# Optimization experiments

Measured on AMD Instinct MI355X. Metric: run time of the kernel, lower is better.

## Reference

```python
import jax, jax.numpy as jnp
import numpy as np

N_NODES = 100000


def _gcn_layer(h, W, b, src, dst, norm, n):
    # h: [N, Fin] -> transform then normalized scatter-add aggregation
    h = h @ W                                   # [N, Fout]
    msg = h[src] * norm[:, None]                # [E', Fout] gather + scale
    out = jax.ops.segment_sum(msg, dst, num_segments=n)  # scatter-add
    return out + b


def setup_inputs() -> dict:
    key = jax.random.key(0)
    k1, k2, k3, k4 = jax.random.split(key, 4)
    N, F_IN, HID, C, E = N_NODES, 512, 128, 40, 1600000
    x = jax.random.normal(k1, (N, F_IN), dtype=jnp.float32)
    edge_index = jax.random.randint(k2, (2, E), 0, N, dtype=jnp.int64)
    W1 = jax.random.normal(k3, (F_IN, HID), dtype=jnp.float32) * (1.0 / np.sqrt(F_IN))
    b1 = jnp.zeros((HID,), dtype=jnp.float32)
    W2 = jax.random.normal(k4, (HID, C), dtype=jnp.float32) * (1.0 / np.sqrt(HID))
    b2 = jnp.zeros((C,), dtype=jnp.float32)
    return {"x": x, "edge_index": edge_index, "W1": W1, "b1": b1, "W2": W2, "b2": b2}


def reference(x, edge_index, W1, b1, W2, b2):
    n = x.shape[0]
    # add self-loops (GCNConv default)
    loop = jnp.arange(n, dtype=edge_index.dtype)
    src = jnp.concatenate([edge_index[0], loop])
    dst = jnp.concatenate([edge_index[1], loop])
    # symmetric normalization: deg counted on destination (in-degree, incl. self-loop)
    deg = jax.ops.segment_sum(jnp.ones_like(dst, dtype=x.dtype), dst, num_segments=n)
    dis = jnp.where(deg > 0, jax.lax.rsqrt(deg), 0.0)  # deg^{-1/2}
    norm = dis[src] * dis[dst]                          # per-edge weight

    h = jax.nn.relu(_gcn_layer(x, W1, b1, src, dst, norm, n))
    # dropout: identity in eval mode (training=False)
    h = _gcn_layer(h, W2, b2, src, dst, norm, n)
    return jax.nn.log_softmax(h, axis=1)
```

## Files before the change

### kernel.cpp

```cpp
#include <hip/hip_runtime.h>
#include <hip/hip_bf16.h>


#define F_IN 512
#define HID  128
#define NC   40
#define NCP  48

typedef __attribute__((ext_vector_type(8))) short bf16x8;
typedef __attribute__((ext_vector_type(4))) float f32x4v;

__device__ __forceinline__ ushort f2bf(float f) {
    unsigned r;
    asm("v_cvt_pk_bf16_f32 %0, %1, %1" : "=v"(r) : "v"(f));
    return (ushort)r;
}
__device__ __forceinline__ unsigned cvtpk(float a, float b) {
    unsigned r;
    asm("v_cvt_pk_bf16_f32 %0, %1, %2" : "=v"(r) : "v"(a), "v"(b));
    return r;
}
__device__ __forceinline__ float bf2f(ushort u) {
    return __uint_as_float((unsigned)u << 16);
}
__device__ __forceinline__ bf16x8 cvt8(float4 lo, float4 hi) {
    union { unsigned u[4]; bf16x8 v; } t;
    t.u[0] = cvtpk(lo.x, lo.y); t.u[1] = cvtpk(lo.z, lo.w);
    t.u[2] = cvtpk(hi.x, hi.y); t.u[3] = cvtpk(hi.z, hi.w);
    return t.v;
}

__global__ void prep_k(const int* __restrict__ dst, int E, int EB,
                       unsigned* __restrict__ cnt,
                       const float* __restrict__ W1, const float* __restrict__ W2,
                       ushort* __restrict__ W1p, ushort* __restrict__ W2p) {
    int b = blockIdx.x;
    if (b < EB) {
        int t = b * 256 + threadIdx.x;
        if (t < E) atomicAdd(&cnt[dst[t]], 1u);
        return;
    }
    int t = (b - EB) * 256 + threadIdx.x;
    if (t < 65536) {
        int j = t & 7, n = (t >> 3) & 127, kb = (t >> 10) & 3, s = t >> 12;
        int k = s * 32 + kb * 8 + j;
        W1p[t] = f2bf(W1[(size_t)k * HID + n]);
    } else {
        int q = t - 65536;
        if (q < 6144) {
            int j = q & 7;
            int i2 = q >> 3;
            int n = i2 % 48;
            int i3 = i2 / 48;
            int kb = i3 & 3, ks = i3 >> 2;
            int k = ks * 32 + kb * 8 + j;
            float v = (n < NC) ? W2[(size_t)k * NC + n] : 0.f;
            W2p[q] = f2bf(v);
        }
    }
}

__global__ __launch_bounds__(1024) void scan_block(const unsigned* __restrict__ cnt,
                                                   unsigned* __restrict__ offs,
                                                   unsigned* __restrict__ bsums,
                                                   float* __restrict__ dis, int N) {
    int tid = threadIdx.x;
    int i = blockIdx.x * 1024 + tid;
    unsigned v = (i < N) ? cnt[i] : 0u;
    if (i < N) dis[i] = rsqrtf((float)v + 1.0f);
    int lane = tid & 63, w = tid >> 6;
    unsigned s = v;
    #pragma unroll
    for (int d = 1; d < 64; d <<= 1) {
        unsigned t = __shfl_up(s, d, 64);
        if (lane >= d) s += t;
    }
    __shared__ unsigned wt[16];
    if (lane == 63) wt[w] = s;
    __syncthreads();
    unsigned add = 0;
    #pragma unroll
    for (int j = 0; j < 16; j++) add += (j < w) ? wt[j] : 0u;
    unsigned incl = s + add;
    if (i < N) offs[i] = incl - v;
    if (tid == 1023) bsums[blockIdx.x] = incl;
}

__global__ __launch_bounds__(1024) void scan_add2(unsigned* __restrict__ offs,
                                                  const unsigned* __restrict__ bsums,
                                                  int N, unsigned total) {
    int i = blockIdx.x * 1024 + threadIdx.x;
    int lane = threadIdx.x & 63;
    unsigned s = 0;
    for (int j = lane; j < (int)blockIdx.x; j += 64) s += bsums[j];
    #pragma unroll
    for (int d = 1; d < 64; d <<= 1) s += __shfl_xor(s, d, 64);
    if (i < N) offs[i] += s;
    if (i == 0) offs[N] = total;
}

__global__ __launch_bounds__(256) void fill_gemm1(
        const int* __restrict__ src, const int* __restrict__ dst,
        const unsigned* __restrict__ offs, unsigned* __restrict__ cursor,
        int* __restrict__ col, int E, int GB,
        const float* __restrict__ A, const ushort* __restrict__ Bp,
        const float* __restrict__ dis, ushort* __restrict__ C, int N) {
    if (blockIdx.x >= GB) {
        int t = (blockIdx.x - GB) * 256 + threadIdx.x;
        if (t < E) {
            int s = src[t], d = dst[t];
            unsigned pos = offs[d] + atomicAdd(&cursor[d], 1u);
            col[pos] = s;
        }
        return;
    }
    const int tid  = threadIdx.x;
    const int wave = tid >> 6;
    const int lane = tid & 63;
    const int quad = lane >> 4;
    const int mr   = lane & 15;
    const int base = (blockIdx.x * 4 + wave) * 32;
    if (base >= N) return;
    const int r0 = base + mr;
    const int r1 = base + 16 + mr;
    const bool ok0 = r0 < N, ok1 = r1 < N;
    const float* ap0 = A + (size_t)(ok0 ? r0 : 0) * F_IN + quad * 8;
    const float* ap1 = A + (size_t)(ok1 ? r1 : 0) * F_IN + quad * 8;
    const ushort* bp = Bp + quad * 1024 + mr * 8;

    f32x4v acc0[8], acc1[8];
    #pragma unroll
    for (int t = 0; t < 8; t++) {
        acc0[t] = (f32x4v){0.f, 0.f, 0.f, 0.f};
        acc1[t] = (f32x4v){0.f, 0.f, 0.f, 0.f};
    }

    float4 av[2][4];
    #pragma unroll
    for (int b = 0; b < 2; b++) {
        av[b][0] = *(const float4*)(ap0 + b * 32);
        av[b][1] = *(const float4*)(ap0 + b * 32 + 4);
        av[b][2] = *(const float4*)(ap1 + b * 32);
        av[b][3] = *(const float4*)(ap1 + b * 32 + 4);
    }

    for (int s = 0; s < 16; s++) {
        bf16x8 fa0 = cvt8(av[s & 1][0], av[s & 1][1]);
        bf16x8 fa1 = cvt8(av[s & 1][2], av[s & 1][3]);
        if (s < 14) {
            av[s & 1][0] = *(const float4*)(ap0 + (s + 2) * 32);
            av[s & 1][1] = *(const float4*)(ap0 + (s + 2) * 32 + 4);
            av[s & 1][2] = *(const float4*)(ap1 + (s + 2) * 32);
            av[s & 1][3] = *(const float4*)(ap1 + (s + 2) * 32 + 4);
        }
        const ushort* bs = bp + s * 4096;
        #pragma unroll
        for (int t = 0; t < 8; t++) {
            bf16x8 b = *(const bf16x8*)(bs + t * 128);
            acc0[t] = __builtin_amdgcn_mfma_f32_16x16x32_bf16(fa0, b, acc0[t], 0, 0, 0);
            acc1[t] = __builtin_amdgcn_mfma_f32_16x16x32_bf16(fa1, b, acc1[t], 0, 0, 0);
        }
    }

    #pragma unroll
    for (int rr = 0; rr < 4; rr++) {
        int ra = base + quad * 4 + rr;
        if (ra < N) {
            float ds = dis[ra];
            #pragma unroll
            for (int t = 0; t < 8; t++)
                C[(size_t)ra * HID + t * 16 + mr] = f2bf(acc0[t][rr] * ds);
        }
        int rb = base + 16 + quad * 4 + rr;
        if (rb < N) {
            float ds = dis[rb];
            #pragma unroll
            for (int t = 0; t < 8; t++)
                C[(size_t)rb * HID + t * 16 + mr] = f2bf(acc1[t][rr] * ds);
        }
    }
}

__global__ __launch_bounds__(256) void agg1_k(const ushort* __restrict__ h,
                                              const int* __restrict__ col,
                                              const unsigned* __restrict__ offs,
                                              const float* __restrict__ dis,
                                              const float* __restrict__ b1,
                                              ushort* __restrict__ out, int N) {
    int node = blockIdx.x * 4 + (threadIdx.x >> 6);
    if (node >= N) return;
    int lane = threadIdx.x & 63;
    int ni = lane >> 4;
    int fl = lane & 15;
    const ushort* hb = h + (size_t)fl * 8;
    float a[8] = {0.f, 0.f, 0.f, 0.f, 0.f, 0.f, 0.f, 0.f};
    if (ni == 0) {
        uint4 v = *(const uint4*)(hb + (size_t)node * HID);
        const ushort* u = (const ushort*)&v;
        #pragma unroll
        for (int j = 0; j < 8; j++) a[j] = bf2f(u[j]);
    }
    unsigned p0 = offs[node], p1 = offs[node + 1];
    int sA = (p0 + ni     < p1) ? col[p0 + ni]     : -1;
    int sB = (p0 + ni + 4 < p1) ? col[p0 + ni + 4] : -1;
    for (unsigned p = p0; p < p1; p += 8) {
        int sC = (p + 8 + ni  < p1) ? col[p + 8 + ni]  : -1;
        int sD = (p + 12 + ni < p1) ? col[p + 12 + ni] : -1;
        if (sA >= 0) {
            uint4 v = *(const uint4*)(hb + (size_t)sA * HID);
            const ushort* u = (const ushort*)&v;
            #pragma unroll
            for (int j = 0; j < 8; j++) a[j] += bf2f(u[j]);
        }
        if (sB >= 0) {
            uint4 v = *(const uint4*)(hb + (size_t)sB * HID);
            const ushort* u = (const ushort*)&v;
            #pragma unroll
            for (int j = 0; j < 8; j++) a[j] += bf2f(u[j]);
        }
        sA = sC; sB = sD;
    }
    #pragma unroll
    for (int j = 0; j < 8; j++) {
        a[j] += __shfl_xor(a[j], 16);
        a[j] += __shfl_xor(a[j], 32);
    }
    if (ni == 0) {
        float dd = dis[node];
        float4 bb0 = *(const float4*)(b1 + fl * 8);
        float4 bb1 = *(const float4*)(b1 + fl * 8 + 4);
        const float bb[8] = {bb0.x, bb0.y, bb0.z, bb0.w, bb1.x, bb1.y, bb1.z, bb1.w};
        __align__(16) ushort o[8];
        #pragma unroll
        for (int j = 0; j < 8; j++) o[j] = f2bf(fmaxf(a[j] * dd + bb[j], 0.f));
        *(uint4*)(out + (size_t)node * HID + (size_t)fl * 8) = *(const uint4*)o;
    }
}

__global__ __launch_bounds__(256) void gemm2_mfma(const ushort* __restrict__ A,
                                                  const ushort* __restrict__ W2p,
                                                  const float* __restrict__ dis,
                                                  ushort* __restrict__ h2, int N) {
    const int tid  = threadIdx.x;
    const int wave = tid >> 6;
    const int lane = tid & 63;
    const int quad = lane >> 4;
    const int mr   = lane & 15;
    const int base = (blockIdx.x * 4 + wave) * 32;
    if (base >= N) return;
    const int r0 = base + mr;
    const int r1 = base + 16 + mr;
    const bool ok0 = r0 < N, ok1 = r1 < N;
    const ushort* ap0 = A + (size_t)(ok0 ? r0 : 0) * HID + quad * 8;
    const ushort* ap1 = A + (size_t)(ok1 ? r1 : 0) * HID + quad * 8;
    const ushort* bp = W2p + quad * 384 + mr * 8;

    f32x4v acc0[3], acc1[3];
    #pragma unroll
    for (int t = 0; t < 3; t++) {
        acc0[t] = (f32x4v){0.f, 0.f, 0.f, 0.f};
        acc1[t] = (f32x4v){0.f, 0.f, 0.f, 0.f};
    }
    #pragma unroll
    for (int ks = 0; ks < 4; ks++) {
        bf16x8 a0 = *(const bf16x8*)(ap0 + ks * 32);
        bf16x8 a1 = *(const bf16x8*)(ap1 + ks * 32);
        #pragma unroll
        for (int t = 0; t < 3; t++) {
            bf16x8 b = *(const bf16x8*)(bp + ks * 1536 + t * 128);
            acc0[t] = __builtin_amdgcn_mfma_f32_16x16x32_bf16(a0, b, acc0[t], 0, 0, 0);
            acc1[t] = __builtin_amdgcn_mfma_f32_16x16x32_bf16(a1, b, acc1[t], 0, 0, 0);
        }
    }
    #pragma unroll
    for (int rr = 0; rr < 4; rr++) {
        int ra = base + quad * 4 + rr;
        if (ra < N) {
            float ds = dis[ra];
            #pragma unroll
            for (int t = 0; t < 3; t++) {
                int c = t * 16 + mr;
                if (c < NC) h2[(size_t)ra * NCP + c] = f2bf(acc0[t][rr] * ds);
            }
        }
        int rb = base + 16 + quad * 4 + rr;
        if (rb < N) {
            float ds = dis[rb];
            #pragma unroll
            for (int t = 0; t < 3; t++) {
                int c = t * 16 + mr;
                if (c < NC) h2[(size_t)rb * NCP + c] = f2bf(acc1[t][rr] * ds);
            }
        }
    }
}

__global__ __launch_bounds__(256) void agg2_ls(const ushort* __restrict__ h2,
                                               const int* __restrict__ col,
                                               const unsigned* __restrict__ offs,
                                               const float* __restrict__ dis,
                                               const float* __restrict__ b2,
                                               float* __restrict__ out, int N) {
    int node = blockIdx.x * 4 + (threadIdx.x >> 6);
    if (node >= N) return;
    int lane = threadIdx.x & 63;
    int ni = lane >> 3;
    int fl = lane & 7;
    const bool act = fl < 5;
    const ushort* hb = h2 + (size_t)fl * 8;
    float a[8] = {0.f, 0.f, 0.f, 0.f, 0.f, 0.f, 0.f, 0.f};
    if (ni == 0 && act) {
        uint4 v = *(const uint4*)(hb + (size_t)node * NCP);
        const ushort* u = (const ushort*)&v;
        #pragma unroll
        for (int j = 0; j < 8; j++) a[j] = bf2f(u[j]);
    }
    unsigned p0 = offs[node], p1 = offs[node + 1];
    int sA = (p0 + ni     < p1) ? col[p0 + ni]     : -1;
    int sB = (p0 + ni + 8 < p1) ? col[p0 + ni + 8] : -1;
    for (unsigned p = p0; p < p1; p += 16) {
        int sC = (p + 16 + ni < p1) ? col[p + 16 + ni] : -1;
        int sD = (p + 24 + ni < p1) ? col[p + 24 + ni] : -1;
        if (sA >= 0 && act) {
            uint4 v = *(const uint4*)(hb + (size_t)sA * NCP);
            const ushort* u = (const ushort*)&v;
            #pragma unroll
            for (int j = 0; j < 8; j++) a[j] += bf2f(u[j]);
        }
        if (sB >= 0 && act) {
            uint4 v = *(const uint4*)(hb + (size_t)sB * NCP);
            const ushort* u = (const ushort*)&v;
            #pragma unroll
            for (int j = 0; j < 8; j++) a[j] += bf2f(u[j]);
        }
        sA = sC; sB = sD;
    }
    #pragma unroll
    for (int j = 0; j < 8; j++) {
        a[j] += __shfl_xor(a[j], 8);
        a[j] += __shfl_xor(a[j], 16);
        a[j] += __shfl_xor(a[j], 32);
    }
    float dd = dis[node];
    float l[8];
    float m = -1e30f;
    if (act) {
        #pragma unroll
        for (int j = 0; j < 8; j++) {
            l[j] = a[j] * dd + b2[fl * 8 + j];
            m = fmaxf(m, l[j]);
        }
    }
    #pragma unroll
    for (int d = 1; d < 8; d <<= 1) m = fmaxf(m, __shfl_xor(m, d, 8));
    float s = 0.f;
    if (act) {
        #pragma unroll
        for (int j = 0; j < 8; j++) s += __expf(l[j] - m);
    }
    #pragma unroll
    for (int d = 1; d < 8; d <<= 1) s += __shfl_xor(s, d, 8);
    float lse = m + __logf(s);
    if (ni == 0 && act) {
        float* op = out + (size_t)node * NC + fl * 8;
        *(float4*)op       = make_float4(l[0]-lse, l[1]-lse, l[2]-lse, l[3]-lse);
        *(float4*)(op + 4) = make_float4(l[4]-lse, l[5]-lse, l[6]-lse, l[7]-lse);
    }
}

extern "C" void kernel_launch(void* const* d_in, const int* in_sizes, int n_in,
                              void* d_out, int out_size, void* d_ws, size_t ws_size,
                              hipStream_t stream) {
    const float* x  = (const float*)d_in[0];
    const int*   ei = (const int*)d_in[1];
    const float* W1 = (const float*)d_in[2];
    const float* b1 = (const float*)d_in[3];
    const float* W2 = (const float*)d_in[4];
    const float* b2 = (const float*)d_in[5];
    float* out = (float*)d_out;

    const int N = in_sizes[0] / F_IN;
    const int E = in_sizes[1] / 2;
    const int* src = ei;
    const int* dst = ei + E;

    char* ws = (char*)d_ws;
    size_t o = 0;
    unsigned* cnt  = (unsigned*)(ws + o); o += (size_t)N * 4;
    unsigned* cur  = (unsigned*)(ws + o); o += (size_t)N * 4;
    float*    dis  = (float*)   (ws + o); o += (size_t)N * 4;
    unsigned* offs = (unsigned*)(ws + o); o += (size_t)(N + 4) * 4;
    unsigned* bsums= (unsigned*)(ws + o); o += 4096;
    int*      col  = (int*)     (ws + o); o += (size_t)E * 4;
    o = (o + 15) & ~(size_t)15;
    ushort*   W1p  = (ushort*)  (ws + o); o += (size_t)F_IN * HID * 2;
    o = (o + 15) & ~(size_t)15;
    ushort*   W2p  = (ushort*)  (ws + o); o += 6144 * 2;
    o = (o + 15) & ~(size_t)15;
    ushort*   h1   = (ushort*)  (ws + o); o += (size_t)N * HID * 2;
    o = (o + 15) & ~(size_t)15;
    ushort*   ag1  = (ushort*)  (ws + o); o += (size_t)N * HID * 2;
    o = (o + 15) & ~(size_t)15;
    ushort*   h2   = (ushort*)  (ws + o); o += (size_t)N * NCP * 2;

    const int nb = (N + 1023) / 1024;
    const int EB = (E + 255) / 256;
    const int PB = (65536 + 6144 + 255) / 256;
    const int GB = (N + 127) / 128;

    hipMemsetAsync(cnt, 0, (size_t)N * 8, stream);
    prep_k<<<EB + PB, 256, 0, stream>>>(dst, E, EB, cnt, W1, W2, W1p, W2p);
    scan_block<<<nb, 1024, 0, stream>>>(cnt, offs, bsums, dis, N);
    scan_add2<<<nb, 1024, 0, stream>>>(offs, bsums, N, (unsigned)E);

    fill_gemm1<<<GB + EB, 256, 0, stream>>>(src, dst, offs, cur, col, E, GB,
                                            x, W1p, dis, h1, N);

    agg1_k<<<(N + 3) / 4, 256, 0, stream>>>(h1, col, offs, dis, b1, ag1, N);

    gemm2_mfma<<<(N + 127) / 128, 256, 0, stream>>>(ag1, W2p, dis, h2, N);
    agg2_ls<<<(N + 3) / 4, 256, 0, stream>>>(h2, col, offs, dis, b2, out, N);
}
```

Baseline: 598.8 us.

## Record per-edge rank during counting and shrink GEMM1 tiles to 16 rows per wave

The degree-count pass now stores each edge's slot (the value returned by the atomic increment), so the CSR fill step writes col directly without a second atomic on a cursor array. This removes the cursor array, halves the memset and drops E contended atomics, at the cost of an extra E-sized rank array written and then read back. Separately, each GEMM1 wave now handles 16 rows instead of 32, with a deeper 4-stage prefetch of A and a fully unrolled k loop. This doubles the GEMM block count and re-reads the packed W1 twice as often per row.

```diff
diff --git a/kernel.cpp b/kernel.cpp
--- a/kernel.cpp
+++ b/kernel.cpp
@@ -31,13 +31,13 @@
 }
 
 __global__ void prep_k(const int* __restrict__ dst, int E, int EB,
-                       unsigned* __restrict__ cnt,
+                       unsigned* __restrict__ cnt, int* __restrict__ rank,
                        const float* __restrict__ W1, const float* __restrict__ W2,
                        ushort* __restrict__ W1p, ushort* __restrict__ W2p) {
     int b = blockIdx.x;
     if (b < EB) {
         int t = b * 256 + threadIdx.x;
-        if (t < E) atomicAdd(&cnt[dst[t]], 1u);
+        if (t < E) rank[t] = (int)atomicAdd(&cnt[dst[t]], 1u);
         return;
     }
     int t = (b - EB) * 256 + threadIdx.x;
@@ -101,16 +101,15 @@
 
 __global__ __launch_bounds__(256) void fill_gemm1(
         const int* __restrict__ src, const int* __restrict__ dst,
-        const unsigned* __restrict__ offs, unsigned* __restrict__ cursor,
+        const unsigned* __restrict__ offs, const int* __restrict__ rank,
         int* __restrict__ col, int E, int GB,
         const float* __restrict__ A, const ushort* __restrict__ Bp,
         const float* __restrict__ dis, ushort* __restrict__ C, int N) {
     if (blockIdx.x >= GB) {
         int t = (blockIdx.x - GB) * 256 + threadIdx.x;
         if (t < E) {
-            int s = src[t], d = dst[t];
-            unsigned pos = offs[d] + atomicAdd(&cursor[d], 1u);
-            col[pos] = s;
+            int d = dst[t];
+            col[offs[d] + (unsigned)rank[t]] = src[t];
         }
         return;
     }
@@ -119,46 +118,36 @@
     const int lane = tid & 63;
     const int quad = lane >> 4;
     const int mr   = lane & 15;
-    const int base = (blockIdx.x * 4 + wave) * 32;
+    const int base = (blockIdx.x * 4 + wave) * 16;
     if (base >= N) return;
     const int r0 = base + mr;
-    const int r1 = base + 16 + mr;
-    const bool ok0 = r0 < N, ok1 = r1 < N;
+    const bool ok0 = r0 < N;
     const float* ap0 = A + (size_t)(ok0 ? r0 : 0) * F_IN + quad * 8;
-    const float* ap1 = A + (size_t)(ok1 ? r1 : 0) * F_IN + quad * 8;
     const ushort* bp = Bp + quad * 1024 + mr * 8;
 
-    f32x4v acc0[8], acc1[8];
-    #pragma unroll
-    for (int t = 0; t < 8; t++) {
-        acc0[t] = (f32x4v){0.f, 0.f, 0.f, 0.f};
-        acc1[t] = (f32x4v){0.f, 0.f, 0.f, 0.f};
-    }
-
-    float4 av[2][4];
-    #pragma unroll
-    for (int b = 0; b < 2; b++) {
+    f32x4v acc0[8];
+    #pragma unroll
+    for (int t = 0; t < 8; t++) acc0[t] = (f32x4v){0.f, 0.f, 0.f, 0.f};
+
+    float4 av[4][2];
+    #pragma unroll
+    for (int b = 0; b < 4; b++) {
         av[b][0] = *(const float4*)(ap0 + b * 32);
         av[b][1] = *(const float4*)(ap0 + b * 32 + 4);
-        av[b][2] = *(const float4*)(ap1 + b * 32);
-        av[b][3] = *(const float4*)(ap1 + b * 32 + 4);
-    }
-
+    }
+
+    #pragma unroll
     for (int s = 0; s < 16; s++) {
-        bf16x8 fa0 = cvt8(av[s & 1][0], av[s & 1][1]);
-        bf16x8 fa1 = cvt8(av[s & 1][2], av[s & 1][3]);
-        if (s < 14) {
-            av[s & 1][0] = *(const float4*)(ap0 + (s + 2) * 32);
-            av[s & 1][1] = *(const float4*)(ap0 + (s + 2) * 32 + 4);
-            av[s & 1][2] = *(const float4*)(ap1 + (s + 2) * 32);
-            av[s & 1][3] = *(const float4*)(ap1 + (s + 2) * 32 + 4);
+        bf16x8 fa0 = cvt8(av[s & 3][0], av[s & 3][1]);
+        if (s < 12) {
+            av[s & 3][0] = *(const float4*)(ap0 + (s + 4) * 32);
+            av[s & 3][1] = *(const float4*)(ap0 + (s + 4) * 32 + 4);
         }
         const ushort* bs = bp + s * 4096;
         #pragma unroll
         for (int t = 0; t < 8; t++) {
             bf16x8 b = *(const bf16x8*)(bs + t * 128);
             acc0[t] = __builtin_amdgcn_mfma_f32_16x16x32_bf16(fa0, b, acc0[t], 0, 0, 0);
-            acc1[t] = __builtin_amdgcn_mfma_f32_16x16x32_bf16(fa1, b, acc1[t], 0, 0, 0);
         }
     }
 
@@ -170,13 +159,6 @@
             #pragma unroll
             for (int t = 0; t < 8; t++)
                 C[(size_t)ra * HID + t * 16 + mr] = f2bf(acc0[t][rr] * ds);
-        }
-        int rb = base + 16 + quad * 4 + rr;
-        if (rb < N) {
-            float ds = dis[rb];
-            #pragma unroll
-            for (int t = 0; t < 8; t++)
-                C[(size_t)rb * HID + t * 16 + mr] = f2bf(acc1[t][rr] * ds);
         }
     }
 }
@@ -387,10 +369,10 @@
     char* ws = (char*)d_ws;
     size_t o = 0;
     unsigned* cnt  = (unsigned*)(ws + o); o += (size_t)N * 4;
-    unsigned* cur  = (unsigned*)(ws + o); o += (size_t)N * 4;
     float*    dis  = (float*)   (ws + o); o += (size_t)N * 4;
     unsigned* offs = (unsigned*)(ws + o); o += (size_t)(N + 4) * 4;
     unsigned* bsums= (unsigned*)(ws + o); o += 4096;
+    int*      rank = (int*)     (ws + o); o += (size_t)E * 4;
     int*      col  = (int*)     (ws + o); o += (size_t)E * 4;
     o = (o + 15) & ~(size_t)15;
     ushort*   W1p  = (ushort*)  (ws + o); o += (size_t)F_IN * HID * 2;
@@ -406,14 +388,14 @@
     const int nb = (N + 1023) / 1024;
     const int EB = (E + 255) / 256;
     const int PB = (65536 + 6144 + 255) / 256;
-    const int GB = (N + 127) / 128;
-
-    hipMemsetAsync(cnt, 0, (size_t)N * 8, stream);
-    prep_k<<<EB + PB, 256, 0, stream>>>(dst, E, EB, cnt, W1, W2, W1p, W2p);
+    const int GB = (N + 63) / 64;
+
+    hipMemsetAsync(cnt, 0, (size_t)N * 4, stream);
+    prep_k<<<EB + PB, 256, 0, stream>>>(dst, E, EB, cnt, rank, W1, W2, W1p, W2p);
     scan_block<<<nb, 1024, 0, stream>>>(cnt, offs, bsums, dis, N);
     scan_add2<<<nb, 1024, 0, stream>>>(offs, bsums, N, (unsigned)E);
 
-    fill_gemm1<<<GB + EB, 256, 0, stream>>>(src, dst, offs, cur, col, E, GB,
+    fill_gemm1<<<GB + EB, 256, 0, stream>>>(src, dst, offs, rank, col, E, GB,
                                             x, W1p, dis, h1, N);
 
     agg1_k<<<(N + 3) / 4, 256, 0, stream>>>(h1, col, offs, dis, b1, ag1, N);
```

Measured after the change: 586.2 us. 2.1% less time.
